# Optimization experiments

Hardware: AMD Instinct MI355X
Metric: run time of the kernel (lower is better)

Reference implementation:

```python
import jax, jax.numpy as jnp
import numpy as np

# Config (matches init_kwargs)
B, DIM = 16, 768
HEADS, DHEAD = 12, 64
H_MEM, W_MEM = 16, 16           # memory grid; N = 256 tokens
MAX_AH, MAX_AW = 3, 3
N = H_MEM * W_MEM


def _area_pool(t):
    """t: [B', N, D] laid out on an H_MEM x W_MEM grid.
    Returns (area_sums [B', M, D], area_sizes [M]) over all rectangle sizes
    (ah, aw) with 1<=ah<=MAX_AH, 1<=aw<=MAX_AW, at every valid position,
    via a 2D integral image (summed-area table)."""
    Bp, _, D = t.shape
    g = t.reshape(Bp, H_MEM, W_MEM, D)
    I = jnp.cumsum(jnp.cumsum(g, axis=1), axis=2)
    I = jnp.pad(I, ((0, 0), (1, 0), (1, 0), (0, 0)))  # [B', H+1, W+1, D]
    sums, sizes = [], []
    for ah in range(1, MAX_AH + 1):
        for aw in range(1, MAX_AW + 1):
            s = (I[:, ah:, aw:] - I[:, :-ah, aw:]
                 - I[:, ah:, :-aw] + I[:, :-ah, :-aw])  # [B', H-ah+1, W-aw+1, D]
            n_pos = s.shape[1] * s.shape[2]
            sums.append(s.reshape(Bp, n_pos, D))
            sizes.append(np.full((n_pos,), float(ah * aw), dtype=np.float32))
    return jnp.concatenate(sums, axis=1), jnp.asarray(np.concatenate(sizes))


def setup_inputs() -> dict:
    key = jax.random.key(0)
    ks = jax.random.split(key, 10)
    s = 0.02
    d = dict(
        x=jax.random.normal(ks[0], (B, N, DIM), jnp.float32),
        # to_qkv: Linear(dim, 3*dim, bias=False); stored as (in, out)
        w_qkv=jax.random.normal(ks[1], (DIM, 3 * DIM), jnp.float32) * s,
        # per-head q/k/v projections (dim -> heads*dim_head) with bias
        w_q=jax.random.normal(ks[2], (DIM, HEADS * DHEAD), jnp.float32) * s,
        b_q=jnp.zeros((HEADS * DHEAD,), jnp.float32),
        w_k=jax.random.normal(ks[3], (DIM, HEADS * DHEAD), jnp.float32) * s,
        b_k=jnp.zeros((HEADS * DHEAD,), jnp.float32),
        w_v=jax.random.normal(ks[4], (DIM, HEADS * DHEAD), jnp.float32) * s,
        b_v=jnp.zeros((HEADS * DHEAD,), jnp.float32),
        # output projection (heads*dim_head -> dim)
        w_o=jax.random.normal(ks[5], (HEADS * DHEAD, DIM), jnp.float32) * s,
        b_o=jnp.zeros((DIM,), jnp.float32),
    )
    return d


def reference(x, w_qkv, w_q, b_q, w_k, b_k, w_v, b_v, w_o, b_o):
    # QKV projection + split: 'b n (qkv d) -> qkv b n d'
    qkv = x @ w_qkv                               # [B, N, 3*DIM]
    q, k, v = jnp.split(qkv, 3, axis=-1)          # each [B, N, DIM]

    def to_heads(t, w, b):                        # 'b n (h d) -> (b h) n d'
        return ((t @ w + b)
                .reshape(B, N, HEADS, DHEAD)
                .transpose(0, 2, 1, 3)
                .reshape(B * HEADS, N, DHEAD))

    qh = to_heads(q, w_q, b_q)
    kh = to_heads(k, w_k, b_k)
    vh = to_heads(v, w_v, b_v)

    # Area keys: mean over each area; area values: sum over each area.
    k_sum, sizes = _area_pool(kh)                 # [BH, M, d], [M]
    k_area = k_sum / sizes[None, :, None]
    v_area, _ = _area_pool(vh)                    # [BH, M, d]

    logits = jnp.einsum('bqd,bmd->bqm', qh, k_area)   # [BH, N, M]
    weights = jax.nn.softmax(logits, axis=-1)
    out = jnp.einsum('bqm,bmd->bqd', weights, v_area)  # [BH, N, d]

    # '(b h) n d -> b n (h d)' then output projection
    out = (out.reshape(B, HEADS, N, DHEAD)
              .transpose(0, 2, 1, 3)
              .reshape(B, N, HEADS * DHEAD))
    return out @ w_o + b_o
```

## Files before the change

kernel.cpp:

```cpp
#include <hip/hip_runtime.h>
#include <hip/hip_bf16.h>

typedef __hip_bfloat16 bf16;
typedef __attribute__((ext_vector_type(8))) short short8b;
typedef __attribute__((ext_vector_type(4))) short short4b;
typedef __attribute__((ext_vector_type(4))) float f32x4;

#define NAREA 2025
#define NAREA_PAD 2048

static __device__ __forceinline__ float b2f(bf16 x) { return __bfloat162float(x); }
static __device__ __forceinline__ short f2bs(float f) {
  bf16 h = __float2bfloat16(f);
  return *(short*)&h;
}

static __device__ __forceinline__ void gll16(const void* g, void* l) {
  __builtin_amdgcn_global_load_lds(
      (const __attribute__((address_space(1))) unsigned int*)(unsigned long long)g,
      (__attribute__((address_space(3))) unsigned int*)(unsigned int)(unsigned long long)l,
      16, 0, 0);
}

__global__ __launch_bounds__(256) void k_prep(
    const float* __restrict__ x, const float* __restrict__ wqkv,
    const float* __restrict__ wq, const float* __restrict__ wk,
    const float* __restrict__ wv,
    bf16* __restrict__ xb, bf16* __restrict__ wqkvb,
    bf16* __restrict__ wqT, bf16* __restrict__ wkT, bf16* __restrict__ wvT,
    int4* __restrict__ rectG, float* __restrict__ invG)
{
  __shared__ float tile[32][33];
  int b = blockIdx.x;
  if (b < 4800) {
    int idx = (b * 256 + threadIdx.x) * 4;
    const int NX = 4096 * 768;
    float4 v;
    bf16* d;
    if (idx < NX) { v = *(const float4*)(x + idx); d = xb + idx; }
    else { v = *(const float4*)(wqkv + (idx - NX)); d = wqkvb + (idx - NX); }
    short4b s = {f2bs(v.x), f2bs(v.y), f2bs(v.z), f2bs(v.w)};
    *(short4b*)d = s;
    return;
  }
  if (b < 6528) {
    int r = b - 4800;
    int z = r / 576; r -= z * 576;
    int by = r / 24, bx = r - by * 24;
    const float* src = (z == 0) ? wq : (z == 1) ? wk : wv;
    bf16* dst = (z == 0) ? wqT : (z == 1) ? wkT : wvT;
    int r0 = by * 32, c0 = bx * 32;
    int lx = threadIdx.x & 31, ly = threadIdx.x >> 5;
#pragma unroll
    for (int yy = 0; yy < 4; ++yy)
      tile[ly + yy * 8][lx] = src[(size_t)(r0 + ly + yy * 8) * 768 + c0 + lx];
    __syncthreads();
#pragma unroll
    for (int yy = 0; yy < 4; ++yy)
      dst[(size_t)(c0 + ly + yy * 8) * 768 + r0 + lx] =
          __float2bfloat16(tile[lx][ly + yy * 8]);
    return;
  }
  int m = (b - 6528) * 256 + threadIdx.x;
  if (m >= NAREA_PAD) return;
  int4 rc = make_int4(0, 0, 0, 0);
  float iv = 0.f;
  if (m < NAREA) {
    int rem = m, ah = 1, aw = 1, found = 0;
    for (int a = 1; a <= 3 && !found; ++a)
      for (int w = 1; w <= 3 && !found; ++w) {
        int np = (17 - a) * (17 - w);
        if (rem < np) { ah = a; aw = w; found = 1; }
        else rem -= np;
      }
    int cw = 17 - aw;
    int y = rem / cw, xx = rem - y * cw;
    rc.x = (y * 17 + xx) * 64;
    rc.y = (y * 17 + (xx + aw)) * 64;
    rc.z = ((y + ah) * 17 + xx) * 64;
    rc.w = ((y + ah) * 17 + (xx + aw)) * 64;
    iv = 1.0f / (float)(ah * aw);
  }
  rectG[m] = rc;
  invG[m] = iv;
}

__global__ __launch_bounds__(256) void k_tcast1(
    const float* __restrict__ src, bf16* __restrict__ dst)
{
  __shared__ float tile[32][33];
  int r0 = blockIdx.y * 32, c0 = blockIdx.x * 32;
  int lx = threadIdx.x & 31, ly = threadIdx.x >> 5;
#pragma unroll
  for (int yy = 0; yy < 4; ++yy)
    tile[ly + yy * 8][lx] = src[(size_t)(r0 + ly + yy * 8) * 768 + c0 + lx];
  __syncthreads();
#pragma unroll
  for (int yy = 0; yy < 4; ++yy)
    dst[(size_t)(c0 + ly + yy * 8) * 768 + r0 + lx] =
        __float2bfloat16(tile[lx][ly + yy * 8]);
}


__global__ __launch_bounds__(256) void k_combine_m(
    const bf16* __restrict__ wqkvb, const bf16* __restrict__ wqT,
    const bf16* __restrict__ wkT, const bf16* __restrict__ wvT,
    bf16* __restrict__ WcTb)
{
  __shared__ __align__(16) short As[2][128 * 32];
  __shared__ __align__(16) short Bs[2][128 * 32];
  const int t3 = blockIdx.z;
  const bf16* BT = (t3 == 0) ? wqT : (t3 == 1) ? wkT : wvT;
  const int m0 = blockIdx.y * 128, n0 = blockIdx.x * 128;
  const int tid = threadIdx.x, lane = tid & 63, w = tid >> 6;
  const int tt = lane & 15, q4 = lane >> 4;
  const int moff = (w & 1) * 64, noff = (w >> 1) * 64;
  const int r_a = tid >> 2, kc = (tid & 3) * 8;

  f32x4 acc[4][4];
#pragma unroll
  for (int i = 0; i < 4; ++i)
#pragma unroll
    for (int j = 0; j < 4; ++j) acc[i][j] = (f32x4){0.f, 0.f, 0.f, 0.f};

#define STAGE_C(k0, buf)                                                        \
  {                                                                             \
    gll16(wqkvb + (size_t)(m0 + r_a) * 2304 + t3 * 768 + (k0) + kc,             \
          &As[buf][w * 512]);                                                   \
    gll16(wqkvb + (size_t)(m0 + r_a + 64) * 2304 + t3 * 768 + (k0) + kc,        \
          &As[buf][2048 + w * 512]);                                            \
    gll16(BT + (size_t)(n0 + r_a) * 768 + (k0) + kc, &Bs[buf][w * 512]);        \
    gll16(BT + (size_t)(n0 + r_a + 64) * 768 + (k0) + kc,                       \
          &Bs[buf][2048 + w * 512]);                                            \
  }

  STAGE_C(0, 0);
  for (int it = 0; it < 24; ++it) {
    __syncthreads();
    if (it < 23) STAGE_C((it + 1) * 32, (it + 1) & 1);
    const short* as = As[it & 1];
    const short* bs = Bs[it & 1];
    short8b afr[4], bfr[4];
#pragma unroll
    for (int mt = 0; mt < 4; ++mt)
      afr[mt] = *(const short8b*)&as[(moff + mt * 16 + tt) * 32 + q4 * 8];
#pragma unroll
    for (int nt = 0; nt < 4; ++nt)
      bfr[nt] = *(const short8b*)&bs[(noff + nt * 16 + tt) * 32 + q4 * 8];
#pragma unroll
    for (int mt = 0; mt < 4; ++mt)
#pragma unroll
      for (int nt = 0; nt < 4; ++nt)
        acc[mt][nt] = __builtin_amdgcn_mfma_f32_16x16x32_bf16(afr[mt], bfr[nt], acc[mt][nt], 0, 0, 0);
  }
#undef STAGE_C

  bf16* C = WcTb + (size_t)t3 * 768 * 768;
#pragma unroll
  for (int nt = 0; nt < 4; ++nt) {
    int n = n0 + noff + nt * 16 + tt;
#pragma unroll
    for (int mt = 0; mt < 4; ++mt) {
      int mb = m0 + moff + mt * 16 + q4 * 4;
      short4b v = {f2bs(acc[mt][nt][0]), f2bs(acc[mt][nt][1]),
                   f2bs(acc[mt][nt][2]), f2bs(acc[mt][nt][3])};
      *(short4b*)&C[(size_t)n * 768 + mb] = v;
    }
  }
}

__global__ __launch_bounds__(256) void k_proj_m(
    const bf16* __restrict__ xb, const bf16* __restrict__ WcTb,
    const float* __restrict__ bq, const float* __restrict__ bk,
    const float* __restrict__ bv,
    bf16* __restrict__ qh, bf16* __restrict__ kh, bf16* __restrict__ vh)
{
  __shared__ __align__(16) short As[2][128 * 32];
  __shared__ __align__(16) short Bs[2][128 * 32];
  const int t3 = blockIdx.z;
  const bf16* BT = WcTb + (size_t)t3 * 768 * 768;
  const float* bias = (t3 == 0) ? bq : (t3 == 1) ? bk : bv;
  bf16* dst = (t3 == 0) ? qh : (t3 == 1) ? kh : vh;
  const int m0 = blockIdx.y * 128, n0 = blockIdx.x * 128;
  const int tid = threadIdx.x, lane = tid & 63, w = tid >> 6;
  const int tt = lane & 15, q4 = lane >> 4;
  const int moff = (w & 1) * 64, noff = (w >> 1) * 64;
  const int r_a = tid >> 2, kc = (tid & 3) * 8;

  f32x4 acc[4][4];
#pragma unroll
  for (int i = 0; i < 4; ++i)
#pragma unroll
    for (int j = 0; j < 4; ++j) acc[i][j] = (f32x4){0.f, 0.f, 0.f, 0.f};

#define STAGE_P(k0, buf)                                                        \
  {                                                                             \
    gll16(xb + (size_t)(m0 + r_a) * 768 + (k0) + kc, &As[buf][w * 512]);        \
    gll16(xb + (size_t)(m0 + r_a + 64) * 768 + (k0) + kc,                       \
          &As[buf][2048 + w * 512]);                                            \
    gll16(BT + (size_t)(n0 + r_a) * 768 + (k0) + kc, &Bs[buf][w * 512]);        \
    gll16(BT + (size_t)(n0 + r_a + 64) * 768 + (k0) + kc,                       \
          &Bs[buf][2048 + w * 512]);                                            \
  }

  STAGE_P(0, 0);
  for (int it = 0; it < 24; ++it) {
    __syncthreads();
    if (it < 23) STAGE_P((it + 1) * 32, (it + 1) & 1);
    const short* as = As[it & 1];
    const short* bs = Bs[it & 1];
    short8b afr[4], bfr[4];
#pragma unroll
    for (int mt = 0; mt < 4; ++mt)
      afr[mt] = *(const short8b*)&as[(moff + mt * 16 + tt) * 32 + q4 * 8];
#pragma unroll
    for (int nt = 0; nt < 4; ++nt)
      bfr[nt] = *(const short8b*)&bs[(noff + nt * 16 + tt) * 32 + q4 * 8];
#pragma unroll
    for (int mt = 0; mt < 4; ++mt)
#pragma unroll
      for (int nt = 0; nt < 4; ++nt)
        acc[mt][nt] = __builtin_amdgcn_mfma_f32_16x16x32_bf16(afr[mt], bfr[nt], acc[mt][nt], 0, 0, 0);
  }
#undef STAGE_P

#pragma unroll
  for (int nt = 0; nt < 4; ++nt) {
    int c = n0 + noff + nt * 16 + tt;
    float bvv = bias[c];
    int h = c >> 6, d = c & 63;
#pragma unroll
    for (int mt = 0; mt < 4; ++mt) {
#pragma unroll
      for (int r = 0; r < 4; ++r) {
        int m = m0 + moff + mt * 16 + q4 * 4 + r;
        dst[(((size_t)((m >> 8) * 12 + h)) << 14) + ((m & 255) << 6) + d] =
            __float2bfloat16(acc[mt][nt][r] + bvv);
      }
    }
  }
}

__global__ __launch_bounds__(256) void k_out_m(
    const bf16* __restrict__ attno, const bf16* __restrict__ woT,
    const float* __restrict__ bo, float* __restrict__ out)
{
  __shared__ __align__(16) short As[2][128 * 32];
  __shared__ __align__(16) short Bs[2][128 * 32];
  const int m0 = blockIdx.y * 128, n0 = blockIdx.x * 128;
  const int tid = threadIdx.x, lane = tid & 63, w = tid >> 6;
  const int tt = lane & 15, q4 = lane >> 4;
  const int moff = (w & 1) * 64, noff = (w >> 1) * 64;
  const int r_a = tid >> 2, kc = (tid & 3) * 8;
  const int m_a0 = m0 + r_a, m_a1 = m0 + r_a + 64;

  f32x4 acc[4][4];
#pragma unroll
  for (int i = 0; i < 4; ++i)
#pragma unroll
    for (int j = 0; j < 4; ++j) acc[i][j] = (f32x4){0.f, 0.f, 0.f, 0.f};

#define STAGE_O(k0, buf)                                                        \
  {                                                                             \
    int k = (k0) + kc;                                                          \
    gll16(attno + (((size_t)((m_a0 >> 8) * 12 + (k >> 6))) << 14) +             \
              ((m_a0 & 255) << 6) + (k & 63),                                   \
          &As[buf][w * 512]);                                                   \
    gll16(attno + (((size_t)((m_a1 >> 8) * 12 + (k >> 6))) << 14) +             \
              ((m_a1 & 255) << 6) + (k & 63),                                   \
          &As[buf][2048 + w * 512]);                                            \
    gll16(woT + (size_t)(n0 + r_a) * 768 + k, &Bs[buf][w * 512]);               \
    gll16(woT + (size_t)(n0 + r_a + 64) * 768 + k, &Bs[buf][2048 + w * 512]);   \
  }

  STAGE_O(0, 0);
  for (int it = 0; it < 24; ++it) {
    __syncthreads();
    if (it < 23) STAGE_O((it + 1) * 32, (it + 1) & 1);
    const short* as = As[it & 1];
    const short* bs = Bs[it & 1];
    short8b afr[4], bfr[4];
#pragma unroll
    for (int mt = 0; mt < 4; ++mt)
      afr[mt] = *(const short8b*)&as[(moff + mt * 16 + tt) * 32 + q4 * 8];
#pragma unroll
    for (int nt = 0; nt < 4; ++nt)
      bfr[nt] = *(const short8b*)&bs[(noff + nt * 16 + tt) * 32 + q4 * 8];
#pragma unroll
    for (int mt = 0; mt < 4; ++mt)
#pragma unroll
      for (int nt = 0; nt < 4; ++nt)
        acc[mt][nt] = __builtin_amdgcn_mfma_f32_16x16x32_bf16(afr[mt], bfr[nt], acc[mt][nt], 0, 0, 0);
  }
#undef STAGE_O

#pragma unroll
  for (int nt = 0; nt < 4; ++nt) {
    int c = n0 + noff + nt * 16 + tt;
    float bvv = bo[c];
#pragma unroll
    for (int mt = 0; mt < 4; ++mt)
#pragma unroll
      for (int r = 0; r < 4; ++r) {
        int m = m0 + moff + mt * 16 + q4 * 4 + r;
        out[(size_t)m * 768 + c] = acc[mt][nt][r] + bvv;
      }
  }
}

__global__ __launch_bounds__(1024) void k_integral_p(
    const bf16* __restrict__ kh, const bf16* __restrict__ vh,
    float* __restrict__ Ik, float* __restrict__ Iv)
{
  __shared__ float sat[17 * 17 * 64];
  int bh = blockIdx.x >> 1;
  bool isv = blockIdx.x & 1;
  const bf16* src = (isv ? vh : kh) + ((size_t)bh << 14);
  float* dst = (isv ? Iv : Ik) + (size_t)bh * 18496;
  int tid = threadIdx.x;
  int d = tid & 63;
  int row = tid >> 6;
  {
    float run = 0.f;
    sat[((row + 1) * 17) * 64 + d] = 0.f;
#pragma unroll
    for (int xx = 0; xx < 16; ++xx) {
      run += b2f(src[(row * 16 + xx) * 64 + d]);
      sat[((row + 1) * 17 + (xx + 1)) * 64 + d] = run;
    }
    if (row == 0) {
#pragma unroll
      for (int xx = 0; xx < 17; ++xx) sat[xx * 64 + d] = 0.f;
    }
  }
  __syncthreads();
  {
    int x = row + 1;
    float run = 0.f;
#pragma unroll
    for (int y = 1; y <= 16; ++y) {
      run += sat[(y * 17 + x) * 64 + d];
      sat[(y * 17 + x) * 64 + d] = run;
    }
  }
  __syncthreads();
  for (int i = tid; i < 18496; i += 1024) dst[i] = sat[i];
}

__global__ __launch_bounds__(1024) void k_attn_m(
    const bf16* __restrict__ qh, const float* __restrict__ Ik,
    const float* __restrict__ Iv, const int4* __restrict__ rectG,
    const float* __restrict__ invG, bf16* __restrict__ attno)
{
  __shared__ __align__(16) short aK2[2][64 * 80];
  __shared__ __align__(16) short aVt2[2][64 * 72];

  const int tid = threadIdx.x;
  const int lane = tid & 63;
  const int w = tid >> 6;
  const int t = lane & 15;
  const int q4 = lane >> 4;
  const int bh = blockIdx.x;
  const int rbase = (t & 12) * 2 + (t & 3);

  const float* Ikb = Ik + (size_t)bh * 18496;
  const float* Ivb = Iv + (size_t)bh * 18496;
  const bf16* qbase = qh + ((size_t)bh << 14);

  short8b qf0 = *(const short8b*)(qbase + (w * 16 + t) * 64 + q4 * 8);
  short8b qf1 = *(const short8b*)(qbase + (w * 16 + t) * 64 + 32 + q4 * 8);

  f32x4 O[4];
#pragma unroll
  for (int i = 0; i < 4; ++i) O[i] = (f32x4){0.f, 0.f, 0.f, 0.f};
  float l = 0.f;

  {
    short* aK = aK2[0];
    short* aVt = aVt2[0];
    short vp[4];
#pragma unroll
    for (int i = 0; i < 4; ++i) {
      int j = w * 4 + i;
      int4 rc = rectG[j];
      float iv = invG[j];
      float kc = Ikb[rc.w + lane] - Ikb[rc.y + lane] - Ikb[rc.z + lane] + Ikb[rc.x + lane];
      float vc = Ivb[rc.w + lane] - Ivb[rc.y + lane] - Ivb[rc.z + lane] + Ivb[rc.x + lane];
      aK[j * 80 + lane] = f2bs(kc * iv);
      vp[i] = f2bs(vc);
    }
    *(short4b*)&aVt[lane * 72 + w * 4] = (short4b){vp[0], vp[1], vp[2], vp[3]};
  }

  float kcr[4], vcr[4], ivr[4];
  for (int it = 0; it < 32; ++it) {
    if (it + 1 < 32) {
      int t0n = (it + 1) * 64;
#pragma unroll
      for (int i = 0; i < 4; ++i) {
        int j = t0n + w * 4 + i;
        int4 rc = rectG[j];
        ivr[i] = invG[j];
        kcr[i] = Ikb[rc.w + lane] - Ikb[rc.y + lane] - Ikb[rc.z + lane] + Ikb[rc.x + lane];
        vcr[i] = Ivb[rc.w + lane] - Ivb[rc.y + lane] - Ivb[rc.z + lane] + Ivb[rc.x + lane];
      }
    }
    __syncthreads();
    const short* aK = aK2[it & 1];
    const short* aVt = aVt2[it & 1];
    if (it + 1 < 32) {
      short* aKn = aK2[(it + 1) & 1];
      short* aVtn = aVt2[(it + 1) & 1];
      short vp[4];
#pragma unroll
      for (int i = 0; i < 4; ++i) {
        aKn[(w * 4 + i) * 80 + lane] = f2bs(kcr[i] * ivr[i]);
        vp[i] = f2bs(vcr[i]);
      }
      *(short4b*)&aVtn[lane * 72 + w * 4] = (short4b){vp[0], vp[1], vp[2], vp[3]};
    }

    const int t0 = it * 64;
    const bool edge = (t0 + 64 > NAREA);
    union { short8b v; unsigned u[4]; } apv[2];
#pragma unroll
    for (int at = 0; at < 4; ++at) {
      int row = rbase + (at & 1) * 4 + (at >> 1) * 32;
      short8b af0 = *(const short8b*)&aK[row * 80 + q4 * 8];
      short8b af1 = *(const short8b*)&aK[row * 80 + 32 + q4 * 8];
      f32x4 s = (f32x4){0.f, 0.f, 0.f, 0.f};
      s = __builtin_amdgcn_mfma_f32_16x16x32_bf16(af0, qf0, s, 0, 0, 0);
      s = __builtin_amdgcn_mfma_f32_16x16x32_bf16(af1, qf1, s, 0, 0, 0);
      int abase = t0 + (at >> 1) * 32 + q4 * 8 + (at & 1) * 4;
      float p[4];
#pragma unroll
      for (int r = 0; r < 4; ++r) {
        p[r] = __expf(s[r]);
        if (edge && (abase + r >= NAREA)) p[r] = 0.f;
      }
      l += (p[0] + p[1]) + (p[2] + p[3]);
      unsigned lo = ((unsigned)(unsigned short)f2bs(p[1]) << 16) |
                    (unsigned short)f2bs(p[0]);
      unsigned hi = ((unsigned)(unsigned short)f2bs(p[3]) << 16) |
                    (unsigned short)f2bs(p[2]);
      apv[at >> 1].u[(at & 1) * 2 + 0] = lo;
      apv[at >> 1].u[(at & 1) * 2 + 1] = hi;
    }
#pragma unroll
    for (int nt = 0; nt < 4; ++nt) {
      short8b vf0 = *(const short8b*)&aVt[(nt * 16 + t) * 72 + q4 * 8];
      short8b vf1 = *(const short8b*)&aVt[(nt * 16 + t) * 72 + 32 + q4 * 8];
      O[nt] = __builtin_amdgcn_mfma_f32_16x16x32_bf16(apv[0].v, vf0, O[nt], 0, 0, 0);
      O[nt] = __builtin_amdgcn_mfma_f32_16x16x32_bf16(apv[1].v, vf1, O[nt], 0, 0, 0);
    }
  }

  l += __shfl_xor(l, 16, 64);
  l += __shfl_xor(l, 32, 64);

  bf16* ob = attno + ((size_t)bh << 14);
#pragma unroll
  for (int r = 0; r < 4; ++r) {
    int qrow = q4 * 4 + r;
    float invl = 1.0f / __shfl(l, qrow, 64);
#pragma unroll
    for (int nt = 0; nt < 4; ++nt)
      ob[(w * 16 + qrow) * 64 + nt * 16 + t] = __float2bfloat16(O[nt][r] * invl);
  }
}

extern "C" void kernel_launch(void* const* d_in, const int* in_sizes, int n_in,
                              void* d_out, int out_size, void* d_ws, size_t ws_size,
                              hipStream_t stream) {
  const float* x    = (const float*)d_in[0];
  const float* wqkv = (const float*)d_in[1];
  const float* wq   = (const float*)d_in[2];
  const float* bq   = (const float*)d_in[3];
  const float* wk   = (const float*)d_in[4];
  const float* bk   = (const float*)d_in[5];
  const float* wv   = (const float*)d_in[6];
  const float* bv   = (const float*)d_in[7];
  const float* wo   = (const float*)d_in[8];
  const float* bo   = (const float*)d_in[9];
  float* out = (float*)d_out;

  char* ws = (char*)d_ws;
  char* ob = (char*)d_out;
  const size_t WC_B = 7077888;
  const size_t QH_B = 6291456;

  bf16* xb    = (bf16*)ob;
  bf16* WcTb  = (bf16*)(ob + QH_B);
  bf16* attno = (bf16*)ws;
  int4*  rectG = (int4*)(ws + QH_B);
  float* invG  = (float*)(ws + QH_B + 32768);
  bf16* qh = (bf16*)(ws + WC_B);
  bf16* kh = (bf16*)(ws + WC_B + QH_B);
  bf16* vh = (bf16*)(ws + WC_B + 2 * QH_B);
  bf16* wqkvb = (bf16*)(ws + WC_B);
  bf16* wqT   = (bf16*)(ws + WC_B + 3538944);
  bf16* wkT   = (bf16*)(ws + WC_B + 4718592);
  bf16* wvT   = (bf16*)(ws + WC_B + 5898240);
  float* Ik = (float*)(ws + WC_B + 3 * QH_B);
  float* Iv = Ik + 3551232;
  bf16* woT = (bf16*)(ws + WC_B + 3 * QH_B);

  k_prep<<<dim3(6536), 256, 0, stream>>>(x, wqkv, wq, wk, wv, xb, wqkvb,
                                         wqT, wkT, wvT, rectG, invG);
  k_combine_m<<<dim3(6, 6, 3), 256, 0, stream>>>(wqkvb, wqT, wkT, wvT, WcTb);
  k_proj_m<<<dim3(6, 32, 3), 256, 0, stream>>>(xb, WcTb, bq, bk, bv, qh, kh, vh);
  k_integral_p<<<dim3(384), 1024, 0, stream>>>(kh, vh, Ik, Iv);
  k_attn_m<<<dim3(192), 1024, 0, stream>>>(qh, Ik, Iv, rectG, invG, attno);
  k_tcast1<<<dim3(24, 24), 256, 0, stream>>>(wo, woT);
  k_out_m<<<dim3(6, 32), 256, 0, stream>>>(attno, woT, bo, out);
}
```

Before: 244.1 us.

## Split attention over area chunks with atomic accumulation and separate normalize kernel

The attention kernel grid grows from one block per batch-head to four, each block handling a quarter of the area tiles, so 768 blocks can fill the GPU instead of 192. Each block atomically adds its unnormalized outputs and softmax denominators into zeroed fp32 buffers. A new elementwise kernel then divides by the summed denominator and writes the bf16 result for the output projection. The cost is two memsets, millions of global float atomics, an extra launch, and recomputing the integral-image prologue for each chunk.

```diff
diff --git a/kernel.cpp b/kernel.cpp
--- a/kernel.cpp
+++ b/kernel.cpp
@@ -350,7 +350,8 @@
 __global__ __launch_bounds__(1024) void k_attn_m(
     const bf16* __restrict__ qh, const float* __restrict__ Ik,
     const float* __restrict__ Iv, const int4* __restrict__ rectG,
-    const float* __restrict__ invG, bf16* __restrict__ attno)
+    const float* __restrict__ invG, float* __restrict__ Oacc,
+    float* __restrict__ lacc)
 {
   __shared__ __align__(16) short aK2[2][64 * 80];
   __shared__ __align__(16) short aVt2[2][64 * 72];
@@ -361,6 +362,7 @@
   const int t = lane & 15;
   const int q4 = lane >> 4;
   const int bh = blockIdx.x;
+  const int it0 = blockIdx.y * 8;
   const int rbase = (t & 12) * 2 + (t & 3);
 
   const float* Ikb = Ik + (size_t)bh * 18496;
@@ -382,8 +384,9 @@
 #pragma unroll
     for (int i = 0; i < 4; ++i) {
       int j = w * 4 + i;
-      int4 rc = rectG[j];
-      float iv = invG[j];
+      int g = it0 * 64 + j;
+      int4 rc = rectG[g];
+      float iv = invG[g];
       float kc = Ikb[rc.w + lane] - Ikb[rc.y + lane] - Ikb[rc.z + lane] + Ikb[rc.x + lane];
       float vc = Ivb[rc.w + lane] - Ivb[rc.y + lane] - Ivb[rc.z + lane] + Ivb[rc.x + lane];
       aK[j * 80 + lane] = f2bs(kc * iv);
@@ -393,8 +396,8 @@
   }
 
   float kcr[4], vcr[4], ivr[4];
-  for (int it = 0; it < 32; ++it) {
-    if (it + 1 < 32) {
+  for (int it = it0; it < it0 + 8; ++it) {
+    if (it + 1 < it0 + 8) {
       int t0n = (it + 1) * 64;
 #pragma unroll
       for (int i = 0; i < 4; ++i) {
@@ -408,7 +411,7 @@
     __syncthreads();
     const short* aK = aK2[it & 1];
     const short* aVt = aVt2[it & 1];
-    if (it + 1 < 32) {
+    if (it + 1 < it0 + 8) {
       short* aKn = aK2[(it + 1) & 1];
       short* aVtn = aVt2[(it + 1) & 1];
       short vp[4];
@@ -458,15 +461,25 @@
   l += __shfl_xor(l, 16, 64);
   l += __shfl_xor(l, 32, 64);
 
-  bf16* ob = attno + ((size_t)bh << 14);
-#pragma unroll
-  for (int r = 0; r < 4; ++r) {
-    int qrow = q4 * 4 + r;
-    float invl = 1.0f / __shfl(l, qrow, 64);
-#pragma unroll
-    for (int nt = 0; nt < 4; ++nt)
-      ob[(w * 16 + qrow) * 64 + nt * 16 + t] = __float2bfloat16(O[nt][r] * invl);
-  }
+  if (q4 == 0) atomicAdd(lacc + (bh << 8) + w * 16 + t, l);
+  float* Ob = Oacc + ((size_t)bh << 14);
+#pragma unroll
+  for (int nt = 0; nt < 4; ++nt)
+#pragma unroll
+    for (int r = 0; r < 4; ++r)
+      atomicAdd(Ob + (w * 16 + q4 * 4 + r) * 64 + nt * 16 + t, O[nt][r]);
+}
+
+__global__ __launch_bounds__(256) void k_norm(
+    const float* __restrict__ Oacc, const float* __restrict__ lacc,
+    bf16* __restrict__ attno)
+{
+  int i = (blockIdx.x * 256 + threadIdx.x) * 4;
+  f32x4 o = *(const f32x4*)(Oacc + i);
+  float invl = 1.0f / lacc[i >> 6];
+  short4b s = {f2bs(o[0] * invl), f2bs(o[1] * invl),
+               f2bs(o[2] * invl), f2bs(o[3] * invl)};
+  *(short4b*)(attno + i) = s;
 }
 
 extern "C" void kernel_launch(void* const* d_in, const int* in_sizes, int n_in,
@@ -491,9 +504,11 @@
 
   bf16* xb    = (bf16*)ob;
   bf16* WcTb  = (bf16*)(ob + QH_B);
+  float* Oacc = (float*)ob;
   bf16* attno = (bf16*)ws;
   int4*  rectG = (int4*)(ws + QH_B);
   float* invG  = (float*)(ws + QH_B + 32768);
+  float* lacc  = (float*)(ws + QH_B + 40960);
   bf16* qh = (bf16*)(ws + WC_B);
   bf16* kh = (bf16*)(ws + WC_B + QH_B);
   bf16* vh = (bf16*)(ws + WC_B + 2 * QH_B);
@@ -509,8 +524,11 @@
                                          wqT, wkT, wvT, rectG, invG);
   k_combine_m<<<dim3(6, 6, 3), 256, 0, stream>>>(wqkvb, wqT, wkT, wvT, WcTb);
   k_proj_m<<<dim3(6, 32, 3), 256, 0, stream>>>(xb, WcTb, bq, bk, bv, qh, kh, vh);
+  hipMemsetAsync(Oacc, 0, 12582912, stream);
+  hipMemsetAsync(lacc, 0, 196608, stream);
   k_integral_p<<<dim3(384), 1024, 0, stream>>>(kh, vh, Ik, Iv);
-  k_attn_m<<<dim3(192), 1024, 0, stream>>>(qh, Ik, Iv, rectG, invG, attno);
+  k_attn_m<<<dim3(192, 4), 1024, 0, stream>>>(qh, Ik, Iv, rectG, invG, Oacc, lacc);
+  k_norm<<<dim3(3072), 256, 0, stream>>>(Oacc, lacc, attno);
   k_tcast1<<<dim3(24, 24), 256, 0, stream>>>(wo, woT);
   k_out_m<<<dim3(6, 32), 256, 0, stream>>>(attno, woT, bo, out);
 }
```

Measured after the change: 275.8 us. 13.0% more time.

## Split area attention across query halves and key halves with a normalize pass

Applied to the files above, without the earlier changes.

The attention kernel now runs on a 192x2x2 grid of 512-thread blocks. Each block takes 128 queries and half of the 2025 areas, and writes unnormalized fp32 partial outputs and row sums. A new k_norm2 kernel adds the two partials, divides by the summed denominators and writes bf16. This is meant to raise the block count above the 256 CUs. The cost is that area key/value construction is repeated for each query half, fp32 partials must be written and read back, and there is one extra launch.

```diff
diff --git a/kernel.cpp b/kernel.cpp
--- a/kernel.cpp
+++ b/kernel.cpp
@@ -347,10 +347,12 @@
   for (int i = tid; i < 18496; i += 1024) dst[i] = sat[i];
 }
 
-__global__ __launch_bounds__(1024) void k_attn_m(
+__global__ __launch_bounds__(512, 6) void k_attn_s(
     const bf16* __restrict__ qh, const float* __restrict__ Ik,
     const float* __restrict__ Iv, const int4* __restrict__ rectG,
-    const float* __restrict__ invG, bf16* __restrict__ attno)
+    const float* __restrict__ invG,
+    float* __restrict__ Op0, float* __restrict__ Op1,
+    float* __restrict__ lp0, float* __restrict__ lp1)
 {
   __shared__ __align__(16) short aK2[2][64 * 80];
   __shared__ __align__(16) short aVt2[2][64 * 72];
@@ -361,14 +363,16 @@
   const int t = lane & 15;
   const int q4 = lane >> 4;
   const int bh = blockIdx.x;
+  const int Q0 = blockIdx.y * 128;
+  const int it0 = blockIdx.z * 16;
   const int rbase = (t & 12) * 2 + (t & 3);
 
   const float* Ikb = Ik + (size_t)bh * 18496;
   const float* Ivb = Iv + (size_t)bh * 18496;
-  const bf16* qbase = qh + ((size_t)bh << 14);
-
-  short8b qf0 = *(const short8b*)(qbase + (w * 16 + t) * 64 + q4 * 8);
-  short8b qf1 = *(const short8b*)(qbase + (w * 16 + t) * 64 + 32 + q4 * 8);
+  const bf16* qrow = qh + ((size_t)bh << 14) + (size_t)(Q0 + w * 16 + t) * 64;
+
+  short8b qf0 = *(const short8b*)(qrow + q4 * 8);
+  short8b qf1 = *(const short8b*)(qrow + 32 + q4 * 8);
 
   f32x4 O[4];
 #pragma unroll
@@ -378,46 +382,48 @@
   {
     short* aK = aK2[0];
     short* aVt = aVt2[0];
-    short vp[4];
-#pragma unroll
-    for (int i = 0; i < 4; ++i) {
-      int j = w * 4 + i;
-      int4 rc = rectG[j];
-      float iv = invG[j];
+    short vp[8];
+#pragma unroll
+    for (int i = 0; i < 8; ++i) {
+      int j = w * 8 + i;
+      int g = it0 * 64 + j;
+      int4 rc = rectG[g];
+      float iv = invG[g];
       float kc = Ikb[rc.w + lane] - Ikb[rc.y + lane] - Ikb[rc.z + lane] + Ikb[rc.x + lane];
       float vc = Ivb[rc.w + lane] - Ivb[rc.y + lane] - Ivb[rc.z + lane] + Ivb[rc.x + lane];
       aK[j * 80 + lane] = f2bs(kc * iv);
       vp[i] = f2bs(vc);
     }
-    *(short4b*)&aVt[lane * 72 + w * 4] = (short4b){vp[0], vp[1], vp[2], vp[3]};
-  }
-
-  float kcr[4], vcr[4], ivr[4];
-  for (int it = 0; it < 32; ++it) {
-    if (it + 1 < 32) {
+    *(short8b*)&aVt[lane * 72 + w * 8] =
+        (short8b){vp[0], vp[1], vp[2], vp[3], vp[4], vp[5], vp[6], vp[7]};
+  }
+
+  float kcr[8], vcr[8];
+  for (int it = it0; it < it0 + 16; ++it) {
+    if (it + 1 < it0 + 16) {
       int t0n = (it + 1) * 64;
 #pragma unroll
-      for (int i = 0; i < 4; ++i) {
-        int j = t0n + w * 4 + i;
+      for (int i = 0; i < 8; ++i) {
+        int j = t0n + w * 8 + i;
         int4 rc = rectG[j];
-        ivr[i] = invG[j];
-        kcr[i] = Ikb[rc.w + lane] - Ikb[rc.y + lane] - Ikb[rc.z + lane] + Ikb[rc.x + lane];
+        kcr[i] = (Ikb[rc.w + lane] - Ikb[rc.y + lane] - Ikb[rc.z + lane] + Ikb[rc.x + lane]) * invG[j];
         vcr[i] = Ivb[rc.w + lane] - Ivb[rc.y + lane] - Ivb[rc.z + lane] + Ivb[rc.x + lane];
       }
     }
     __syncthreads();
     const short* aK = aK2[it & 1];
     const short* aVt = aVt2[it & 1];
-    if (it + 1 < 32) {
+    if (it + 1 < it0 + 16) {
       short* aKn = aK2[(it + 1) & 1];
       short* aVtn = aVt2[(it + 1) & 1];
-      short vp[4];
-#pragma unroll
-      for (int i = 0; i < 4; ++i) {
-        aKn[(w * 4 + i) * 80 + lane] = f2bs(kcr[i] * ivr[i]);
+      short vp[8];
+#pragma unroll
+      for (int i = 0; i < 8; ++i) {
+        aKn[(w * 8 + i) * 80 + lane] = f2bs(kcr[i]);
         vp[i] = f2bs(vcr[i]);
       }
-      *(short4b*)&aVtn[lane * 72 + w * 4] = (short4b){vp[0], vp[1], vp[2], vp[3]};
+      *(short8b*)&aVtn[lane * 72 + w * 8] =
+          (short8b){vp[0], vp[1], vp[2], vp[3], vp[4], vp[5], vp[6], vp[7]};
     }
 
     const int t0 = it * 64;
@@ -458,15 +464,30 @@
   l += __shfl_xor(l, 16, 64);
   l += __shfl_xor(l, 32, 64);
 
-  bf16* ob = attno + ((size_t)bh << 14);
-#pragma unroll
-  for (int r = 0; r < 4; ++r) {
-    int qrow = q4 * 4 + r;
-    float invl = 1.0f / __shfl(l, qrow, 64);
-#pragma unroll
-    for (int nt = 0; nt < 4; ++nt)
-      ob[(w * 16 + qrow) * 64 + nt * 16 + t] = __float2bfloat16(O[nt][r] * invl);
-  }
+  float* lp = blockIdx.z ? lp1 : lp0;
+  float* Op = blockIdx.z ? Op1 : Op0;
+  if (q4 == 0) lp[(bh << 8) + Q0 + w * 16 + t] = l;
+  float* Ob = Op + (((size_t)(bh << 8) + Q0 + w * 16) << 6);
+#pragma unroll
+  for (int nt = 0; nt < 4; ++nt)
+#pragma unroll
+    for (int r = 0; r < 4; ++r)
+      Ob[(q4 * 4 + r) * 64 + nt * 16 + t] = O[nt][r];
+}
+
+__global__ __launch_bounds__(256) void k_norm2(
+    const float* __restrict__ Op0, const float* __restrict__ Op1,
+    const float* __restrict__ lp0, const float* __restrict__ lp1,
+    bf16* __restrict__ attno)
+{
+  int i = (blockIdx.x * 256 + threadIdx.x) * 4;
+  f32x4 a = *(const f32x4*)(Op0 + i);
+  f32x4 b = *(const f32x4*)(Op1 + i);
+  int q = i >> 6;
+  float invl = 1.0f / (lp0[q] + lp1[q]);
+  short4b s = {f2bs((a[0] + b[0]) * invl), f2bs((a[1] + b[1]) * invl),
+               f2bs((a[2] + b[2]) * invl), f2bs((a[3] + b[3]) * invl)};
+  *(short4b*)(attno + i) = s;
 }
 
 extern "C" void kernel_launch(void* const* d_in, const int* in_sizes, int n_in,
@@ -491,12 +512,16 @@
 
   bf16* xb    = (bf16*)ob;
   bf16* WcTb  = (bf16*)(ob + QH_B);
+  float* Op0  = (float*)ob;
   bf16* attno = (bf16*)ws;
   int4*  rectG = (int4*)(ws + QH_B);
   float* invG  = (float*)(ws + QH_B + 32768);
+  float* lp0   = (float*)(ws + QH_B + 40960);
+  float* lp1   = lp0 + 49152;
   bf16* qh = (bf16*)(ws + WC_B);
   bf16* kh = (bf16*)(ws + WC_B + QH_B);
   bf16* vh = (bf16*)(ws + WC_B + 2 * QH_B);
+  float* Op1 = (float*)(ws + WC_B + QH_B);
   bf16* wqkvb = (bf16*)(ws + WC_B);
   bf16* wqT   = (bf16*)(ws + WC_B + 3538944);
   bf16* wkT   = (bf16*)(ws + WC_B + 4718592);
@@ -510,7 +535,9 @@
   k_combine_m<<<dim3(6, 6, 3), 256, 0, stream>>>(wqkvb, wqT, wkT, wvT, WcTb);
   k_proj_m<<<dim3(6, 32, 3), 256, 0, stream>>>(xb, WcTb, bq, bk, bv, qh, kh, vh);
   k_integral_p<<<dim3(384), 1024, 0, stream>>>(kh, vh, Ik, Iv);
-  k_attn_m<<<dim3(192), 1024, 0, stream>>>(qh, Ik, Iv, rectG, invG, attno);
+  k_attn_s<<<dim3(192, 2, 2), 512, 0, stream>>>(qh, Ik, Iv, rectG, invG,
+                                                Op0, Op1, lp0, lp1);
+  k_norm2<<<dim3(3072), 256, 0, stream>>>(Op0, Op1, lp0, lp1, attno);
   k_tcast1<<<dim3(24, 24), 256, 0, stream>>>(wo, woT);
   k_out_m<<<dim3(6, 32), 256, 0, stream>>>(attno, woT, bo, out);
 }
```

New measurement: 281.1 us. 15.1% more time.

## Precompute area keys/values in bf16 and run MFMA attention over them

Applied to the files above, without the earlier changes.

Adds a kernel that builds the summed-area table in shared memory and writes every area key (mean) and transposed area value (sum) to global memory in bf16. A new attention kernel streams these tiles through double-buffered LDS and does QK and PV with MFMA, using exp without max subtraction. This removes the per-tile integral-image gathers from the attention loop, at the cost of roughly 100 MB of extra workspace traffic. The old path is kept as a fallback when the workspace is too small.

```diff
diff --git a/kernel.cpp b/kernel.cpp
--- a/kernel.cpp
+++ b/kernel.cpp
@@ -305,6 +305,176 @@
         int m = m0 + moff + mt * 16 + q4 * 4 + r;
         out[(size_t)m * 768 + c] = acc[mt][nt][r] + bvv;
       }
+  }
+}
+
+__global__ __launch_bounds__(1024) void k_area_pre(
+    const bf16* __restrict__ kh, const bf16* __restrict__ vh,
+    const int4* __restrict__ rectG, const float* __restrict__ invG,
+    bf16* __restrict__ Karea, bf16* __restrict__ VareaT)
+{
+  __shared__ float sat[17 * 17 * 64];
+  int bh = blockIdx.x >> 1;
+  bool isv = blockIdx.x & 1;
+  const bf16* src = (isv ? vh : kh) + ((size_t)bh << 14);
+  int tid = threadIdx.x;
+  int d = tid & 63;
+  int row = tid >> 6;
+  {
+    float run = 0.f;
+    sat[((row + 1) * 17) * 64 + d] = 0.f;
+#pragma unroll
+    for (int xx = 0; xx < 16; ++xx) {
+      run += b2f(src[(row * 16 + xx) * 64 + d]);
+      sat[((row + 1) * 17 + (xx + 1)) * 64 + d] = run;
+    }
+    if (row == 0) {
+#pragma unroll
+      for (int xx = 0; xx < 17; ++xx) sat[xx * 64 + d] = 0.f;
+    }
+  }
+  __syncthreads();
+  {
+    int x = row + 1;
+    float run = 0.f;
+#pragma unroll
+    for (int y = 1; y <= 16; ++y) {
+      run += sat[(y * 17 + x) * 64 + d];
+      sat[(y * 17 + x) * 64 + d] = run;
+    }
+  }
+  __syncthreads();
+  if (!isv) {
+    int mrow = tid >> 3;
+    int d0 = (tid & 7) * 8;
+    bf16* out = Karea + ((size_t)bh << 17);
+    for (int s = 0; s < 16; ++s) {
+      int m = s * 128 + mrow;
+      int4 rc = rectG[m];
+      float iv = invG[m];
+      short v[8];
+#pragma unroll
+      for (int j = 0; j < 8; ++j) {
+        int dd = d0 + j;
+        float df = sat[rc.w + dd] - sat[rc.y + dd] - sat[rc.z + dd] + sat[rc.x + dd];
+        v[j] = f2bs(df * iv);
+      }
+      *(short8b*)&out[((size_t)m << 6) + d0] =
+          (short8b){v[0], v[1], v[2], v[3], v[4], v[5], v[6], v[7]};
+    }
+  } else {
+    int mcol = tid & 63;
+    int r16 = tid >> 6;
+    bf16* out = VareaT + ((size_t)bh << 17);
+    for (int s = 0; s < 128; ++s) {
+      int idx = s * 16 + r16;
+      int it = idx >> 6, dd = idx & 63;
+      int4 rc = rectG[it * 64 + mcol];
+      float df = sat[rc.w + dd] - sat[rc.y + dd] - sat[rc.z + dd] + sat[rc.x + dd];
+      out[(((size_t)it << 6) + dd) * 64 + mcol] = __float2bfloat16(df);
+    }
+  }
+}
+
+__global__ __launch_bounds__(512) void k_attn_f(
+    const bf16* __restrict__ qh, const bf16* __restrict__ Karea,
+    const bf16* __restrict__ VareaT, bf16* __restrict__ attno)
+{
+  __shared__ __align__(16) short aK2[2][64 * 80];
+  __shared__ __align__(16) short aVt2[2][64 * 80];
+
+  const int tid = threadIdx.x;
+  const int lane = tid & 63;
+  const int w = tid >> 6;
+  const int t = lane & 15;
+  const int q4 = lane >> 4;
+  const int bh = blockIdx.x;
+  const int Q0 = blockIdx.y * 128;
+  const int rbase = (t & 12) * 2 + (t & 3);
+
+  const bf16* Kb = Karea + ((size_t)bh << 17);
+  const bf16* Vb = VareaT + ((size_t)bh << 17);
+  const bf16* qrow = qh + ((size_t)bh << 14) + (size_t)(Q0 + w * 16 + t) * 64;
+
+  short8b qf0 = *(const short8b*)(qrow + q4 * 8);
+  short8b qf1 = *(const short8b*)(qrow + 32 + q4 * 8);
+
+  f32x4 O[4];
+#pragma unroll
+  for (int i = 0; i < 4; ++i) O[i] = (f32x4){0.f, 0.f, 0.f, 0.f};
+  float l = 0.f;
+
+  const int a8 = tid >> 3;
+  const int c8 = (tid & 7) * 8;
+
+  {
+    short8b k0 = *(const short8b*)&Kb[((size_t)a8 << 6) + c8];
+    short8b v0 = *(const short8b*)&Vb[((size_t)a8 << 6) + c8];
+    *(short8b*)&aK2[0][a8 * 80 + c8] = k0;
+    *(short8b*)&aVt2[0][a8 * 80 + c8] = v0;
+  }
+
+  for (int it = 0; it < 32; ++it) {
+    short8b kn, vn;
+    if (it + 1 < 32) {
+      size_t off = ((size_t)((it + 1) * 64 + a8) << 6) + c8;
+      kn = *(const short8b*)&Kb[off];
+      vn = *(const short8b*)&Vb[off];
+    }
+    __syncthreads();
+    const short* aK = aK2[it & 1];
+    const short* aVt = aVt2[it & 1];
+    if (it + 1 < 32) {
+      *(short8b*)&aK2[(it + 1) & 1][a8 * 80 + c8] = kn;
+      *(short8b*)&aVt2[(it + 1) & 1][a8 * 80 + c8] = vn;
+    }
+
+    const int t0 = it * 64;
+    const bool edge = (t0 + 64 > NAREA);
+    union { short8b v; unsigned u[4]; } apv[2];
+#pragma unroll
+    for (int at = 0; at < 4; ++at) {
+      int row = rbase + (at & 1) * 4 + (at >> 1) * 32;
+      short8b af0 = *(const short8b*)&aK[row * 80 + q4 * 8];
+      short8b af1 = *(const short8b*)&aK[row * 80 + 32 + q4 * 8];
+      f32x4 s = (f32x4){0.f, 0.f, 0.f, 0.f};
+      s = __builtin_amdgcn_mfma_f32_16x16x32_bf16(af0, qf0, s, 0, 0, 0);
+      s = __builtin_amdgcn_mfma_f32_16x16x32_bf16(af1, qf1, s, 0, 0, 0);
+      int abase = t0 + (at >> 1) * 32 + q4 * 8 + (at & 1) * 4;
+      float p[4];
+#pragma unroll
+      for (int r = 0; r < 4; ++r) {
+        p[r] = __expf(s[r]);
+        if (edge && (abase + r >= NAREA)) p[r] = 0.f;
+      }
+      l += (p[0] + p[1]) + (p[2] + p[3]);
+      unsigned lo = ((unsigned)(unsigned short)f2bs(p[1]) << 16) |
+                    (unsigned short)f2bs(p[0]);
+      unsigned hi = ((unsigned)(unsigned short)f2bs(p[3]) << 16) |
+                    (unsigned short)f2bs(p[2]);
+      apv[at >> 1].u[(at & 1) * 2 + 0] = lo;
+      apv[at >> 1].u[(at & 1) * 2 + 1] = hi;
+    }
+#pragma unroll
+    for (int nt = 0; nt < 4; ++nt) {
+      short8b vf0 = *(const short8b*)&aVt[(nt * 16 + t) * 80 + q4 * 8];
+      short8b vf1 = *(const short8b*)&aVt[(nt * 16 + t) * 80 + 32 + q4 * 8];
+      O[nt] = __builtin_amdgcn_mfma_f32_16x16x32_bf16(apv[0].v, vf0, O[nt], 0, 0, 0);
+      O[nt] = __builtin_amdgcn_mfma_f32_16x16x32_bf16(apv[1].v, vf1, O[nt], 0, 0, 0);
+    }
+  }
+
+  l += __shfl_xor(l, 16, 64);
+  l += __shfl_xor(l, 32, 64);
+
+  bf16* ob = attno + ((size_t)bh << 14);
+#pragma unroll
+  for (int r = 0; r < 4; ++r) {
+    int qr = q4 * 4 + r;
+    float invl = 1.0f / __shfl(l, qr, 64);
+#pragma unroll
+    for (int nt = 0; nt < 4; ++nt)
+      ob[(Q0 + w * 16 + qr) * 64 + nt * 16 + t] = __float2bfloat16(O[nt][r] * invl);
   }
 }
 
@@ -488,6 +658,7 @@
   char* ob = (char*)d_out;
   const size_t WC_B = 7077888;
   const size_t QH_B = 6291456;
+  const size_t AREA_B = 50331648;
 
   bf16* xb    = (bf16*)ob;
   bf16* WcTb  = (bf16*)(ob + QH_B);
@@ -501,16 +672,26 @@
   bf16* wqT   = (bf16*)(ws + WC_B + 3538944);
   bf16* wkT   = (bf16*)(ws + WC_B + 4718592);
   bf16* wvT   = (bf16*)(ws + WC_B + 5898240);
+  bf16* Karea  = (bf16*)(ws + WC_B + 3 * QH_B);
+  bf16* VareaT = (bf16*)(ws + WC_B + 3 * QH_B + AREA_B);
   float* Ik = (float*)(ws + WC_B + 3 * QH_B);
   float* Iv = Ik + 3551232;
   bf16* woT = (bf16*)(ws + WC_B + 3 * QH_B);
+
+  const size_t REQ = WC_B + 3 * QH_B + 2 * AREA_B;
+  const bool primary = (ws_size >= REQ);
 
   k_prep<<<dim3(6536), 256, 0, stream>>>(x, wqkv, wq, wk, wv, xb, wqkvb,
                                          wqT, wkT, wvT, rectG, invG);
   k_combine_m<<<dim3(6, 6, 3), 256, 0, stream>>>(wqkvb, wqT, wkT, wvT, WcTb);
   k_proj_m<<<dim3(6, 32, 3), 256, 0, stream>>>(xb, WcTb, bq, bk, bv, qh, kh, vh);
-  k_integral_p<<<dim3(384), 1024, 0, stream>>>(kh, vh, Ik, Iv);
-  k_attn_m<<<dim3(192), 1024, 0, stream>>>(qh, Ik, Iv, rectG, invG, attno);
+  if (primary) {
+    k_area_pre<<<dim3(384), 1024, 0, stream>>>(kh, vh, rectG, invG, Karea, VareaT);
+    k_attn_f<<<dim3(192, 2), 512, 0, stream>>>(qh, Karea, VareaT, attno);
+  } else {
+    k_integral_p<<<dim3(384), 1024, 0, stream>>>(kh, vh, Ik, Iv);
+    k_attn_m<<<dim3(192), 1024, 0, stream>>>(qh, Ik, Iv, rectG, invG, attno);
+  }
   k_tcast1<<<dim3(24, 24), 256, 0, stream>>>(wo, woT);
   k_out_m<<<dim3(6, 32), 256, 0, stream>>>(attno, woT, bo, out);
 }
```

After: 637.7 us. 161% more time.
